# Optimization experiments

Hardware: AMD Instinct MI355X
Metric: run time of the kernel (lower is better)

Reference implementation:

```python
import jax, jax.numpy as jnp
import numpy as np

N = 8192
NHID = 256

def setup_inputs() -> dict:
    key = jax.random.key(0)
    k1, k2, k3 = jax.random.split(key, 3)
    x = jax.random.normal(k1, (N, NHID), dtype=jnp.float32)
    # dense (row-normalized-ish) adjacency; values in [0,1)
    adj = jax.random.uniform(k2, (N, N), dtype=jnp.float32) / N
    W = jax.random.normal(k3, (NHID, NHID), dtype=jnp.float32) * (1.0 / np.sqrt(NHID))
    b = jnp.zeros((NHID,), dtype=jnp.float32)
    return {"x": x, "adj": adj, "W": W, "b": b}

def reference(x, adj, W, b):
    # GCN layer: adj @ (x W) + b, then ReLU (dropout is identity at inference)
    support = x @ W + b            # [N, nhid]
    h = adj @ support              # [N, nhid]  (sparse-style aggregation, dense here)
    h = jax.nn.relu(h)
    # outer-product structure reconstruction
    return h @ h.T                 # [N, N]
```

## Files before the change

kernel.cpp:

```cpp
#include <hip/hip_runtime.h>
#include <hip/hip_bf16.h>
#include <stdint.h>

#define GLOBAL_AS __attribute__((address_space(1)))
#define LDS_AS    __attribute__((address_space(3)))

typedef __attribute__((ext_vector_type(8))) short          short8;
typedef __attribute__((ext_vector_type(4))) float          floatx4;
typedef __attribute__((ext_vector_type(4))) unsigned short ushort4v;

static __device__ __forceinline__ unsigned short f2bf_bits(float f) {
    union { float f; unsigned int u; } v; v.f = f;
    unsigned int r = v.u + 0x7FFFu + ((v.u >> 16) & 1u);
    return (unsigned short)(r >> 16);
}

static __device__ __forceinline__ floatx4 mfma16(short8 a, short8 b, floatx4 c) {
    return __builtin_amdgcn_mfma_f32_16x16x32_bf16(a, b, c, 0, 0, 0);
}

template<int BM, int BN, int BK, int WM, int WN, bool A_F32, bool B_F32, int EPI>
__global__ __launch_bounds__(256, 2)
void gemm_bt(const void* __restrict__ Ap, const void* __restrict__ Bp,
             const float* __restrict__ bias, void* __restrict__ Cp,
             int lda, int ldb, int ldc, int klen, long pstride)
{
    constexpr int NWM = BM / WM;
    constexpr int NWN = BN / WN;
    static_assert(NWM * NWN == 4, "4 waves per block");
    constexpr int FM = WM / 16;
    constexpr int FN = WN / 16;

    __shared__ __align__(16) unsigned short As[BM * BK];
    __shared__ __align__(16) unsigned short Bs[BN * BK];

    const int tid  = threadIdx.x;
    const int lane = tid & 63;
    const int wave = tid >> 6;
    const int wm   = (wave % NWM) * WM;
    const int wn   = (wave / NWM) * WN;
    const int quad = lane >> 4;
    const int l16  = lane & 15;
    const long m0 = (long)blockIdx.x * BM;
    const long n0 = (long)blockIdx.y * BN;
    const long k0 = (long)blockIdx.z * (long)klen;

    floatx4 acc[FM][FN];
#pragma unroll
    for (int i = 0; i < FM; ++i)
#pragma unroll
        for (int j = 0; j < FN; ++j) {
            floatx4 z = {0.f, 0.f, 0.f, 0.f};
            acc[i][j] = z;
        }

    for (int kk = 0; kk < klen; kk += BK) {
        {
            constexpr int CH = BM * BK / 8;
            if constexpr (A_F32) {
                const float* A = (const float*)Ap;
#pragma unroll
                for (int c0 = 0; c0 < CH; c0 += 256) {
                    int c   = c0 + tid;
                    int row = c / (BK / 8);
                    int col = (c % (BK / 8)) * 8;
                    const float* src = A + (m0 + row) * (long)lda + (k0 + kk + col);
                    floatx4 f0 = *(const floatx4*)(src);
                    floatx4 f1 = *(const floatx4*)(src + 4);
                    union { unsigned short u[8]; short8 v; } pk;
                    pk.u[0] = f2bf_bits(f0.x); pk.u[1] = f2bf_bits(f0.y);
                    pk.u[2] = f2bf_bits(f0.z); pk.u[3] = f2bf_bits(f0.w);
                    pk.u[4] = f2bf_bits(f1.x); pk.u[5] = f2bf_bits(f1.y);
                    pk.u[6] = f2bf_bits(f1.z); pk.u[7] = f2bf_bits(f1.w);
                    *(short8*)&As[c * 8] = pk.v;
                }
            } else {
                const unsigned short* A = (const unsigned short*)Ap;
#pragma unroll
                for (int c0 = 0; c0 < CH; c0 += 256) {
                    int c   = c0 + tid;
                    int row = c / (BK / 8);
                    int col = (c % (BK / 8)) * 8;
                    const unsigned short* src = A + (m0 + row) * (long)lda + (k0 + kk + col);
                    __builtin_amdgcn_global_load_lds((const GLOBAL_AS unsigned int*)src,
                                                     (LDS_AS unsigned int*)&As[c * 8],
                                                     16, 0, 0);
                }
            }
        }
        {
            constexpr int CH = BN * BK / 8;
            if constexpr (B_F32) {
                const float* B = (const float*)Bp;
#pragma unroll
                for (int c0 = 0; c0 < CH; c0 += 256) {
                    int c   = c0 + tid;
                    int row = c / (BK / 8);
                    int col = (c % (BK / 8)) * 8;
                    const float* src = B + (n0 + row) * (long)ldb + (k0 + kk + col);
                    floatx4 f0 = *(const floatx4*)(src);
                    floatx4 f1 = *(const floatx4*)(src + 4);
                    union { unsigned short u[8]; short8 v; } pk;
                    pk.u[0] = f2bf_bits(f0.x); pk.u[1] = f2bf_bits(f0.y);
                    pk.u[2] = f2bf_bits(f0.z); pk.u[3] = f2bf_bits(f0.w);
                    pk.u[4] = f2bf_bits(f1.x); pk.u[5] = f2bf_bits(f1.y);
                    pk.u[6] = f2bf_bits(f1.z); pk.u[7] = f2bf_bits(f1.w);
                    *(short8*)&Bs[c * 8] = pk.v;
                }
            } else {
                const unsigned short* B = (const unsigned short*)Bp;
#pragma unroll
                for (int c0 = 0; c0 < CH; c0 += 256) {
                    int c   = c0 + tid;
                    int row = c / (BK / 8);
                    int col = (c % (BK / 8)) * 8;
                    const unsigned short* src = B + (n0 + row) * (long)ldb + (k0 + kk + col);
                    __builtin_amdgcn_global_load_lds((const GLOBAL_AS unsigned int*)src,
                                                     (LDS_AS unsigned int*)&Bs[c * 8],
                                                     16, 0, 0);
                }
            }
        }
        __syncthreads();

#pragma unroll
        for (int ks = 0; ks < BK; ks += 32) {
            short8 af[FM], bfr[FN];
#pragma unroll
            for (int i = 0; i < FM; ++i)
                af[i] = *(const short8*)&As[(wm + i * 16 + l16) * BK + ks + quad * 8];
#pragma unroll
            for (int j = 0; j < FN; ++j)
                bfr[j] = *(const short8*)&Bs[(wn + j * 16 + l16) * BK + ks + quad * 8];
#pragma unroll
            for (int i = 0; i < FM; ++i)
#pragma unroll
                for (int j = 0; j < FN; ++j)
                    acc[i][j] = mfma16(af[i], bfr[j], acc[i][j]);
        }
        __syncthreads();
    }

#pragma unroll
    for (int i = 0; i < FM; ++i)
#pragma unroll
        for (int j = 0; j < FN; ++j)
#pragma unroll
            for (int v = 0; v < 4; ++v) {
                long r = m0 + wm + i * 16 + quad * 4 + v;
                long c = n0 + wn + j * 16 + l16;
                float val = acc[i][j][v];
                if constexpr (EPI == 0) {
                    val += bias[r];
                    ((unsigned short*)Cp)[r * (long)ldc + c] = f2bf_bits(val);
                } else if constexpr (EPI == 2) {
                    ((float*)Cp)[r * (long)ldc + c] = val;
                } else {
                    ((float*)Cp)[(long)blockIdx.z * pstride + r * (long)ldc + c] = val;
                }
            }
}

template<int BM, int BN, int BK, int WM, int WN>
__global__ __launch_bounds__(256, 2)
void gemm_sym(const unsigned short* __restrict__ A, float* __restrict__ C,
              int ld, int ldc, int klen)
{
    constexpr int NWM = BM / WM;
    constexpr int NWN = BN / WN;
    static_assert(NWM * NWN == 4, "4 waves per block");
    constexpr int FM = WM / 16;
    constexpr int FN = WN / 16;

    __shared__ __align__(16) unsigned short As[BM * BK];
    __shared__ __align__(16) unsigned short Bs[BN * BK];

    const int kblk = blockIdx.x;
    int bi = (int)((sqrtf(8.f * (float)kblk + 1.f) - 1.f) * 0.5f);
    while ((bi + 1) * (bi + 2) / 2 <= kblk) ++bi;
    while (bi * (bi + 1) / 2 > kblk) --bi;
    const int bj = kblk - bi * (bi + 1) / 2;

    const long m0 = (long)bi * BM;
    const long n0 = (long)bj * BN;

    const int tid  = threadIdx.x;
    const int lane = tid & 63;
    const int wave = tid >> 6;
    const int wm   = (wave % NWM) * WM;
    const int wn   = (wave / NWM) * WN;
    const int quad = lane >> 4;
    const int l16  = lane & 15;

    floatx4 acc[FM][FN];
#pragma unroll
    for (int i = 0; i < FM; ++i)
#pragma unroll
        for (int j = 0; j < FN; ++j) {
            floatx4 z = {0.f, 0.f, 0.f, 0.f};
            acc[i][j] = z;
        }

    for (int kk = 0; kk < klen; kk += BK) {
        {
            constexpr int CH = BM * BK / 8;
#pragma unroll
            for (int c0 = 0; c0 < CH; c0 += 256) {
                int c   = c0 + tid;
                int row = c / (BK / 8);
                int col = (c % (BK / 8)) * 8;
                const unsigned short* src = A + (m0 + row) * (long)ld + (kk + col);
                __builtin_amdgcn_global_load_lds((const GLOBAL_AS unsigned int*)src,
                                                 (LDS_AS unsigned int*)&As[c * 8],
                                                 16, 0, 0);
            }
        }
        {
            constexpr int CH = BN * BK / 8;
#pragma unroll
            for (int c0 = 0; c0 < CH; c0 += 256) {
                int c   = c0 + tid;
                int row = c / (BK / 8);
                int col = (c % (BK / 8)) * 8;
                const unsigned short* src = A + (n0 + row) * (long)ld + (kk + col);
                __builtin_amdgcn_global_load_lds((const GLOBAL_AS unsigned int*)src,
                                                 (LDS_AS unsigned int*)&Bs[c * 8],
                                                 16, 0, 0);
            }
        }
        __syncthreads();

#pragma unroll
        for (int ks = 0; ks < BK; ks += 32) {
            short8 af[FM], bfr[FN];
#pragma unroll
            for (int i = 0; i < FM; ++i)
                af[i] = *(const short8*)&As[(wm + i * 16 + l16) * BK + ks + quad * 8];
#pragma unroll
            for (int j = 0; j < FN; ++j)
                bfr[j] = *(const short8*)&Bs[(wn + j * 16 + l16) * BK + ks + quad * 8];
#pragma unroll
            for (int i = 0; i < FM; ++i)
#pragma unroll
                for (int j = 0; j < FN; ++j)
                    acc[i][j] = mfma16(af[i], bfr[j], acc[i][j]);
        }
        __syncthreads();
    }

#pragma unroll
    for (int i = 0; i < FM; ++i)
#pragma unroll
        for (int j = 0; j < FN; ++j) {
            const long r0 = m0 + wm + i * 16 + quad * 4;
            const long c  = n0 + wn + j * 16 + l16;
#pragma unroll
            for (int v = 0; v < 4; ++v)
                C[(r0 + v) * (long)ldc + c] = acc[i][j][v];
            if (bi != bj)
                *(floatx4*)&C[c * (long)ldc + r0] = acc[i][j];
        }
}

__global__ void transpose_w_kernel(const float* __restrict__ W, unsigned short* __restrict__ Wt)
{
    int idx = blockIdx.x * 256 + threadIdx.x;
    int n = idx >> 8;
    int k = idx & 255;
    Wt[n * 256 + k] = f2bf_bits(W[k * 256 + n]);
}

__global__ void reduce_relu_kernel(const float* __restrict__ parts, long pstride, int nparts,
                                   unsigned short* __restrict__ h)
{
    int i = (blockIdx.x * 256 + threadIdx.x) * 4;
    floatx4 s = *(const floatx4*)(parts + i);
    for (int p = 1; p < nparts; ++p) {
        floatx4 t = *(const floatx4*)(parts + (long)p * pstride + i);
        s.x += t.x; s.y += t.y; s.z += t.z; s.w += t.w;
    }
    ushort4v o;
    o.x = f2bf_bits(fmaxf(s.x, 0.f));
    o.y = f2bf_bits(fmaxf(s.y, 0.f));
    o.z = f2bf_bits(fmaxf(s.z, 0.f));
    o.w = f2bf_bits(fmaxf(s.w, 0.f));
    *(ushort4v*)&h[i] = o;
}

extern "C" void kernel_launch(void* const* d_in, const int* in_sizes, int n_in,
                              void* d_out, int out_size, void* d_ws, size_t ws_size,
                              hipStream_t stream)
{
    const float* x   = (const float*)d_in[0];
    const float* adj = (const float*)d_in[1];
    const float* W   = (const float*)d_in[2];
    const float* b   = (const float*)d_in[3];
    float* out = (float*)d_out;

    char* ws = (char*)d_ws;
    const long PSTRIDE = 8192L * 256L;

    const size_t BIG_NEED = 8519680u + 8u * 8388608u;
    const bool big = ws_size >= BIG_NEED;

    if (big) {
        unsigned short* Wt   = (unsigned short*)(ws);
        unsigned short* supT = (unsigned short*)(ws + 131072);
        unsigned short* h    = (unsigned short*)(ws + 4325376);
        float*          parts= (float*)         (ws + 8519680);

        transpose_w_kernel<<<256, 256, 0, stream>>>(W, Wt);

        gemm_bt<32, 256, 64, 32, 64, false, true, 0>
            <<<dim3(8, 32, 1), 256, 0, stream>>>(Wt, x, b, supT, 256, 256, 8192, 256, 0);

        gemm_bt<128, 256, 64, 64, 128, true, false, 3>
            <<<dim3(64, 1, 8), 256, 0, stream>>>(adj, supT, nullptr, parts,
                                                 8192, 8192, 256, 1024, PSTRIDE);

        reduce_relu_kernel<<<2048, 256, 0, stream>>>(parts, PSTRIDE, 8, h);

        gemm_sym<128, 128, 64, 64, 64>
            <<<dim3(2080, 1, 1), 256, 0, stream>>>(h, out, 256, 8192, 256);
    } else {
        unsigned short* Wt   = (unsigned short*)(ws);
        unsigned short* supT = (unsigned short*)(ws + 131072);
        unsigned short* h    = (unsigned short*)(ws + 4325376);
        float*          parts= (float*)         (ws + 8519680);

        transpose_w_kernel<<<256, 256, 0, stream>>>(W, Wt);

        gemm_bt<32, 256, 64, 32, 64, false, true, 0>
            <<<dim3(8, 32, 1), 256, 0, stream>>>(Wt, x, b, supT, 256, 256, 8192, 256, 0);

        gemm_bt<32, 256, 64, 32, 64, true, false, 3>
            <<<dim3(256, 1, 2), 256, 0, stream>>>(adj, supT, nullptr, parts,
                                                  8192, 8192, 256, 4096, PSTRIDE);

        reduce_relu_kernel<<<2048, 256, 0, stream>>>(parts, PSTRIDE, 2, h);

        gemm_sym<128, 128, 64, 64, 64>
            <<<dim3(2080, 1, 1), 256, 0, stream>>>(h, out, 256, 8192, 256);
    }
}
```

Before: 582.3 us.

## Add double-buffered adj aggregation GEMM with async B loads to LDS

Replaces the generic split-K GEMM for adj @ support with a dedicated kernel that uses 64x256 tiles, BK=32 and double-buffered LDS. The support operand is streamed straight into LDS with global_load_lds, while the next fp32 adj tile is loaded into registers and converted to bf16 during the current tile's MFMA work. The grid doubles to 128x8 blocks, which is meant to raise occupancy and hide the latency of reading the large fp32 adj matrix. In exchange the code is more specialized, with hardcoded sizes, and the smaller tile reloads the support operand more often.

New measurement: 579.3 us. No clear change (-0.5%).

```diff
diff --git a/kernel.cpp b/kernel.cpp
--- a/kernel.cpp
+++ b/kernel.cpp
@@ -161,6 +161,117 @@
             }
 }
 
+template<int SPLITK>
+__global__ __launch_bounds__(256, 2)
+void gemm_adj(const float* __restrict__ A, const unsigned short* __restrict__ B,
+              float* __restrict__ P, long pstride)
+{
+    constexpr int BM = 64, BN = 256, BK = 32;
+    constexpr int KLEN = 8192 / SPLITK;
+    constexpr int NT = KLEN / BK;
+
+    __shared__ __align__(16) unsigned short As[2][BM * BK];
+    __shared__ __align__(16) unsigned short Bs[2][BN * BK];
+
+    const int tid  = threadIdx.x;
+    const int lane = tid & 63;
+    const int wave = tid >> 6;
+    const int wn   = wave * 64;
+    const int quad = lane >> 4;
+    const int l16  = lane & 15;
+    const long m0 = (long)blockIdx.x * BM;
+    const long k0 = (long)blockIdx.z * (long)KLEN;
+
+    const int arow = tid >> 2;
+    const int acol = (tid & 3) * 8;
+    const float* aptr = A + (m0 + arow) * 8192L + (k0 + acol);
+
+    floatx4 acc[4][4];
+#pragma unroll
+    for (int i = 0; i < 4; ++i)
+#pragma unroll
+        for (int j = 0; j < 4; ++j) {
+            floatx4 z = {0.f, 0.f, 0.f, 0.f};
+            acc[i][j] = z;
+        }
+
+    {
+        floatx4 f0 = *(const floatx4*)(aptr);
+        floatx4 f1 = *(const floatx4*)(aptr + 4);
+#pragma unroll
+        for (int i = 0; i < 4; ++i) {
+            int c = tid + i * 256;
+            const unsigned short* src = B + (long)(c >> 2) * 8192L + (k0 + (c & 3) * 8);
+            __builtin_amdgcn_global_load_lds((const GLOBAL_AS unsigned int*)src,
+                                             (LDS_AS unsigned int*)&Bs[0][c * 8],
+                                             16, 0, 0);
+        }
+        union { unsigned short u[8]; short8 v; } pk;
+        pk.u[0] = f2bf_bits(f0.x); pk.u[1] = f2bf_bits(f0.y);
+        pk.u[2] = f2bf_bits(f0.z); pk.u[3] = f2bf_bits(f0.w);
+        pk.u[4] = f2bf_bits(f1.x); pk.u[5] = f2bf_bits(f1.y);
+        pk.u[6] = f2bf_bits(f1.z); pk.u[7] = f2bf_bits(f1.w);
+        *(short8*)&As[0][tid * 8] = pk.v;
+        __syncthreads();
+    }
+
+    for (int t = 0; t < NT; ++t) {
+        const int cur = t & 1;
+        const int nxt = cur ^ 1;
+        const bool pf = (t + 1 < NT);
+
+        floatx4 f0, f1;
+        if (pf) {
+            const float* ap = aptr + (t + 1) * BK;
+            f0 = *(const floatx4*)(ap);
+            f1 = *(const floatx4*)(ap + 4);
+#pragma unroll
+            for (int i = 0; i < 4; ++i) {
+                int c = tid + i * 256;
+                const unsigned short* src =
+                    B + (long)(c >> 2) * 8192L + (k0 + (long)(t + 1) * BK + (c & 3) * 8);
+                __builtin_amdgcn_global_load_lds((const GLOBAL_AS unsigned int*)src,
+                                                 (LDS_AS unsigned int*)&Bs[nxt][c * 8],
+                                                 16, 0, 0);
+            }
+        }
+
+        short8 af[4], bfr[4];
+#pragma unroll
+        for (int i = 0; i < 4; ++i)
+            af[i] = *(const short8*)&As[cur][(i * 16 + l16) * BK + quad * 8];
+#pragma unroll
+        for (int j = 0; j < 4; ++j)
+            bfr[j] = *(const short8*)&Bs[cur][(wn + j * 16 + l16) * BK + quad * 8];
+#pragma unroll
+        for (int i = 0; i < 4; ++i)
+#pragma unroll
+            for (int j = 0; j < 4; ++j)
+                acc[i][j] = mfma16(af[i], bfr[j], acc[i][j]);
+
+        if (pf) {
+            union { unsigned short u[8]; short8 v; } pk;
+            pk.u[0] = f2bf_bits(f0.x); pk.u[1] = f2bf_bits(f0.y);
+            pk.u[2] = f2bf_bits(f0.z); pk.u[3] = f2bf_bits(f0.w);
+            pk.u[4] = f2bf_bits(f1.x); pk.u[5] = f2bf_bits(f1.y);
+            pk.u[6] = f2bf_bits(f1.z); pk.u[7] = f2bf_bits(f1.w);
+            *(short8*)&As[nxt][tid * 8] = pk.v;
+        }
+        __syncthreads();
+    }
+
+#pragma unroll
+    for (int i = 0; i < 4; ++i)
+#pragma unroll
+        for (int j = 0; j < 4; ++j)
+#pragma unroll
+            for (int v = 0; v < 4; ++v) {
+                long r = m0 + i * 16 + quad * 4 + v;
+                long c = wn + j * 16 + l16;
+                P[(long)blockIdx.z * pstride + r * 256L + c] = acc[i][j][v];
+            }
+}
+
 template<int BM, int BN, int BK, int WM, int WN>
 __global__ __launch_bounds__(256, 2)
 void gemm_sym(const unsigned short* __restrict__ A, float* __restrict__ C,
@@ -314,9 +425,7 @@
         gemm_bt<32, 256, 64, 32, 64, false, true, 0>
             <<<dim3(8, 32, 1), 256, 0, stream>>>(Wt, x, b, supT, 256, 256, 8192, 256, 0);
 
-        gemm_bt<128, 256, 64, 64, 128, true, false, 3>
-            <<<dim3(64, 1, 8), 256, 0, stream>>>(adj, supT, nullptr, parts,
-                                                 8192, 8192, 256, 1024, PSTRIDE);
+        gemm_adj<8><<<dim3(128, 1, 8), 256, 0, stream>>>(adj, supT, parts, PSTRIDE);
 
         reduce_relu_kernel<<<2048, 256, 0, stream>>>(parts, PSTRIDE, 8, h);
 
```
